# Kernel tuning notes

Measured on AMD Instinct MI355X. Metric: run time of the kernel, lower is better.

Reference implementation:

```python
import jax, jax.numpy as jnp
import numpy as np

B, S, H, L, V = 128, 512, 1024, 4, 32000


def setup_inputs() -> dict:
    key = jax.random.key(0)
    ks = jax.random.split(key, 7)
    lengths = jax.random.randint(ks[0], (B,), 1, S + 1)
    lengths = lengths.at[0].set(S)  # force max length == S so T is static
    tok = jax.random.randint(ks[1], (B, S), 1, V)  # nonzero tokens inside length
    pos = jnp.arange(S)[None, :]
    x = jnp.where(pos < lengths[:, None], tok, 0)  # 0 = pad (x>0 defines length)
    emb = jax.random.normal(ks[2], (V, H), dtype=jnp.float32) * 0.02
    W_ih = jax.random.normal(ks[3], (L, 4 * H, H), dtype=jnp.float32) / np.float32(np.sqrt(H))
    W_hh = jax.random.normal(ks[4], (L, 4 * H, H), dtype=jnp.float32) / np.float32(np.sqrt(H))
    b_ih = jax.random.normal(ks[5], (L, 4 * H), dtype=jnp.float32) * 0.01
    b_hh = jax.random.normal(ks[6], (L, 4 * H), dtype=jnp.float32) * 0.01
    return {"x": x, "emb": emb, "W_ih": W_ih, "W_hh": W_hh, "b_ih": b_ih, "b_hh": b_hh}


def reference(x, emb, W_ih, W_hh, b_ih, b_hh):
    # lengths and pack's descending sort (pack_padded_sequence, enforce_sorted=False)
    lengths = jnp.sum(x > 0, axis=1)                         # [B]
    sorted_idx = jnp.argsort(-lengths, stable=True)          # sorted (desc) order
    unsort_idx = jnp.argsort(sorted_idx)                     # packed.unsorted_indices

    # Source bug: `start` is never advanced, so every iteration runs a ONE-step
    # stacked LSTM (zero init state) on packed.data[0:bs_t] == t=0 embeddings of
    # the bs_t longest sequences. Compute that single step once on all rows.
    xt = emb[x[sorted_idx, 0]]                               # [B, H] sorted order
    h0 = jnp.zeros_like(xt)                                  # zero initial hidden
    hs, cs = [], []
    for l in range(W_ih.shape[0]):
        gates = xt @ W_ih[l].T + b_ih[l] + h0 @ W_hh[l].T + b_hh[l]
        i, f, g, o = jnp.split(gates, 4, axis=-1)            # torch LSTMCell order
        c = jax.nn.sigmoid(i) * jnp.tanh(g)                  # f * c0 = 0
        h = jax.nn.sigmoid(o) * jnp.tanh(c)
        xt = h
        hs.append(h)
        cs.append(c)

    # output[t, b] = top-layer h for original seq b, zeroed where t >= lengths[b]
    T = x.shape[1]                                           # max length == S
    h_top = xt[unsort_idx]                                   # back to original order
    tmask = (jnp.arange(T)[:, None] < lengths[None, :]).astype(h_top.dtype)  # [T,B]
    output = tmask[:, :, None] * h_top[None, :, :]           # [T, B, H]

    # state from the LAST loop iteration: sorted order, rows >= bs_last zero-padded
    bs_last = jnp.sum(lengths >= T)                          # batch size at t = T-1
    smask = (jnp.arange(x.shape[0]) < bs_last).astype(h_top.dtype)[None, :, None]
    state_h = jnp.stack(hs, axis=0) * smask                  # [L, B, H]
    state_c = jnp.stack(cs, axis=0) * smask                  # [L, B, H]
    return output, state_h, state_c
```

## Files before the change

kernel.cpp:

```cpp
#include <hip/hip_runtime.h>

#define Bn 128
#define Sn 512
#define Hn 1024
#define Ln 4

typedef float nfloat4 __attribute__((ext_vector_type(4)));

__device__ __forceinline__ float sigmoidf_(float x) { return 1.0f / (1.0f + __expf(-x)); }

__global__ __launch_bounds__(1024) void lensort_kernel(const int* __restrict__ x,
                                                       int* __restrict__ lengths,
                                                       int* __restrict__ rank,
                                                       int* __restrict__ tok_sorted,
                                                       int* __restrict__ bs_last) {
  __shared__ int pc[128][8];
  __shared__ int sl[128];
  __shared__ int cnt;
  const int t = threadIdx.x;
  const int row = t >> 3, seg = t & 7;
  int c = 0;
  const int4* xp = (const int4*)x + row * 128 + seg * 16;
#pragma unroll
  for (int i = 0; i < 16; i++) {
    int4 v = xp[i];
    c += (v.x > 0) + (v.y > 0) + (v.z > 0) + (v.w > 0);
  }
  pc[row][seg] = c;
  if (t == 0) cnt = 0;
  __syncthreads();
  int len = 0;
  if (t < 128) {
#pragma unroll
    for (int i = 0; i < 8; i++) len += pc[t][i];
    sl[t] = len;
    lengths[t] = len;
  }
  __syncthreads();
  if (t < 128) {
    int r = 0;
    for (int b2 = 0; b2 < 128; b2++) {
      int l2 = sl[b2];
      r += (l2 > len) || (l2 == len && b2 < t);
    }
    rank[t] = r;
    tok_sorted[r] = x[t * Sn];
    if (len >= Sn) atomicAdd(&cnt, 1);
  }
  __syncthreads();
  if (t == 0) bs_last[0] = cnt;
}

__global__ __launch_bounds__(320) void gemm_kernel(const float* __restrict__ xt,
                                                   const int* __restrict__ tok,
                                                   const float* __restrict__ Wl,
                                                   float* __restrict__ part,
                                                   const int* __restrict__ lengths,
                                                   float* __restrict__ out,
                                                   const int layer) {
  __shared__ float xtT[32][132];
  __shared__ float Ws[32][96];
  __shared__ int sTok[128];
  const int t = threadIdx.x;
  const int mtile = blockIdx.x & 31;
  const int kc = blockIdx.x >> 5;

  if (tok != nullptr) {
    if (t < 128) sTok[t] = tok[t];
    __syncthreads();
  }

  if (t >= 256) {
    const int lane = t - 256;
    const int b = blockIdx.x & 127;
    const int half = blockIdx.x >> 7;
    const int len = lengths[b];
    const int tw0 = 32 + layer * 120 + half * 60;
    const nfloat4 z = (nfloat4)0.0f;
#pragma unroll
    for (int tile = 0; tile < 4; tile++) {
      __builtin_amdgcn_s_barrier();
      const int r0 = tw0 + tile * 15;
      for (int i = 0; i < 15; i++) {
        const int tt = r0 + i;
        if (tt >= len) {
          nfloat4* p = (nfloat4*)out + ((size_t)tt * 128 + b) * 256 + lane * 4;
          __builtin_nontemporal_store(z, p + 0);
          __builtin_nontemporal_store(z, p + 1);
          __builtin_nontemporal_store(z, p + 2);
          __builtin_nontemporal_store(z, p + 3);
        }
      }
      __builtin_amdgcn_s_barrier();
    }
    return;
  }

  const int rg = t & 31;
  const int msub = t >> 5;
  const int k0 = kc * 128;
  const int kv4 = (t & 7) * 4;

  const float* xrow[4];
#pragma unroll
  for (int i = 0; i < 4; i++) {
    const int r = i * 32 + (t >> 3);
    const int row = (tok != nullptr) ? sTok[r] : r;
    xrow[i] = xt + (size_t)row * 1024;
  }

  float acc[3][4][4];
#pragma unroll
  for (int q = 0; q < 3; q++)
#pragma unroll
    for (int mm = 0; mm < 4; mm++)
#pragma unroll
      for (int rr = 0; rr < 4; rr++) acc[q][mm][rr] = 0.0f;

  float4 xreg[4], wreg[3];
  {
#pragma unroll
    for (int i = 0; i < 4; i++) xreg[i] = *(const float4*)&xrow[i][k0 + kv4];
#pragma unroll
    for (int i = 0; i < 3; i++) {
      int jj = i * 32 + (t >> 3);
      int q = jj >> 5, mloc = jj & 31;
      int qoff = (q == 0) ? 0 : ((q == 1) ? 2048 : 3072);
      wreg[i] = *(const float4*)&Wl[(size_t)(qoff + mtile * 32 + mloc) * 1024 + k0 + kv4];
    }
  }

#pragma unroll
  for (int tile = 0; tile < 4; tile++) {
    __syncthreads();
#pragma unroll
    for (int i = 0; i < 4; i++) {
      const int r = i * 32 + (t >> 3);
      xtT[kv4 + 0][r] = xreg[i].x;
      xtT[kv4 + 1][r] = xreg[i].y;
      xtT[kv4 + 2][r] = xreg[i].z;
      xtT[kv4 + 3][r] = xreg[i].w;
    }
#pragma unroll
    for (int i = 0; i < 3; i++) {
      const int jj = i * 32 + (t >> 3);
      Ws[kv4 + 0][jj] = wreg[i].x;
      Ws[kv4 + 1][jj] = wreg[i].y;
      Ws[kv4 + 2][jj] = wreg[i].z;
      Ws[kv4 + 3][jj] = wreg[i].w;
    }
    float4 xnxt[4], wnxt[3];
    if (tile < 3) {
      const int kt = k0 + (tile + 1) * 32;
#pragma unroll
      for (int i = 0; i < 4; i++) xnxt[i] = *(const float4*)&xrow[i][kt + kv4];
#pragma unroll
      for (int i = 0; i < 3; i++) {
        int jj = i * 32 + (t >> 3);
        int q = jj >> 5, mloc = jj & 31;
        int qoff = (q == 0) ? 0 : ((q == 1) ? 2048 : 3072);
        wnxt[i] = *(const float4*)&Wl[(size_t)(qoff + mtile * 32 + mloc) * 1024 + kt + kv4];
      }
    }
    __syncthreads();
#pragma unroll
    for (int kk = 0; kk < 32; kk++) {
      const float4 xv = *(const float4*)&xtT[kk][rg * 4];
      const float4 w0 = *(const float4*)&Ws[kk][msub * 4];
      const float4 w1 = *(const float4*)&Ws[kk][32 + msub * 4];
      const float4 w2 = *(const float4*)&Ws[kk][64 + msub * 4];
      const float xa[4] = {xv.x, xv.y, xv.z, xv.w};
      const float wv[3][4] = {{w0.x, w0.y, w0.z, w0.w},
                              {w1.x, w1.y, w1.z, w1.w},
                              {w2.x, w2.y, w2.z, w2.w}};
#pragma unroll
      for (int q = 0; q < 3; q++)
#pragma unroll
        for (int mm = 0; mm < 4; mm++)
#pragma unroll
          for (int rr = 0; rr < 4; rr++)
            acc[q][mm][rr] = fmaf(wv[q][mm], xa[rr], acc[q][mm][rr]);
    }
    if (tile < 3) {
#pragma unroll
      for (int i = 0; i < 4; i++) xreg[i] = xnxt[i];
#pragma unroll
      for (int i = 0; i < 3; i++) wreg[i] = wnxt[i];
    }
  }

  const int mbase = mtile * 32 + msub * 4;
#pragma unroll
  for (int q = 0; q < 3; q++)
#pragma unroll
    for (int mm = 0; mm < 4; mm++) {
      float4 v = make_float4(acc[q][mm][0], acc[q][mm][1], acc[q][mm][2], acc[q][mm][3]);
      *(float4*)&part[(((size_t)kc * 3 + q) * 1024 + (mbase + mm)) * 128 + rg * 4] = v;
    }
}

__global__ __launch_bounds__(128) void act_kernel(const float* __restrict__ part,
                                                  const float* __restrict__ bih,
                                                  const float* __restrict__ bhh,
                                                  const int* __restrict__ bs_last,
                                                  float* __restrict__ xt_out,
                                                  float* __restrict__ sh,
                                                  float* __restrict__ sc) {
  const int r = threadIdx.x;
  const int m0 = blockIdx.x * 4;
  const int bs = bs_last[0];
  float hv[4], cv[4];
#pragma unroll
  for (int mm = 0; mm < 4; mm++) {
    const int m = m0 + mm;
    float si = 0.f, sg = 0.f, so = 0.f;
#pragma unroll
    for (int kc = 0; kc < 8; kc++) {
      const float* p = part + (((size_t)kc * 3) * 1024 + m) * 128 + r;
      si += p[0];
      sg += p[(size_t)1024 * 128];
      so += p[(size_t)2048 * 128];
    }
    si += bih[m] + bhh[m];
    sg += bih[2048 + m] + bhh[2048 + m];
    so += bih[3072 + m] + bhh[3072 + m];
    const float c = sigmoidf_(si) * tanhf(sg);
    const float h = sigmoidf_(so) * tanhf(c);
    hv[mm] = h;
    cv[mm] = c;
  }
  const float msk = (r < bs) ? 1.0f : 0.0f;
  *(float4*)&xt_out[(size_t)r * 1024 + m0] = make_float4(hv[0], hv[1], hv[2], hv[3]);
  *(float4*)&sh[(size_t)r * 1024 + m0] =
      make_float4(msk * hv[0], msk * hv[1], msk * hv[2], msk * hv[3]);
  *(float4*)&sc[(size_t)r * 1024 + m0] =
      make_float4(msk * cv[0], msk * cv[1], msk * cv[2], msk * cv[3]);
}

__global__ __launch_bounds__(256) void bcast_kernel(const float* __restrict__ hfin,
                                                    const int* __restrict__ lengths,
                                                    const int* __restrict__ rank,
                                                    float* __restrict__ out) {
  const int b = blockIdx.x & 127;
  const int c = blockIdx.x >> 7;
  const int len = lengths[b];
  const int t0 = c * 64;
  if (t0 < len) {
    const nfloat4 v = ((const nfloat4*)hfin)[rank[b] * 256 + threadIdx.x];
    const int hi = (len < t0 + 64) ? len : (t0 + 64);
    nfloat4* p = (nfloat4*)out + ((size_t)t0 * 128 + b) * 256 + threadIdx.x;
    for (int tt = t0; tt < hi; tt++) {
      __builtin_nontemporal_store(v, p);
      p += 32768;
    }
  }
  if (c == 0 && len < 32) {
    const nfloat4 z = (nfloat4)0.0f;
    nfloat4* pz = (nfloat4*)out + ((size_t)len * 128 + b) * 256 + threadIdx.x;
    for (int tt = len; tt < 32; tt++) {
      __builtin_nontemporal_store(z, pz);
      pz += 32768;
    }
  }
}

extern "C" void kernel_launch(void* const* d_in, const int* in_sizes, int n_in,
                              void* d_out, int out_size, void* d_ws, size_t ws_size,
                              hipStream_t stream) {
  const int* x = (const int*)d_in[0];
  const float* emb = (const float*)d_in[1];
  const float* W_ih = (const float*)d_in[2];
  const float* b_ih = (const float*)d_in[4];
  const float* b_hh = (const float*)d_in[5];

  float* out = (float*)d_out;
  float* sh = out + (size_t)Sn * Bn * Hn;
  float* sc = sh + (size_t)Ln * Bn * Hn;
  float* part = out;

  char* ws = (char*)d_ws;
  int* lengths = (int*)ws;
  int* rank = lengths + 128;
  int* tok_sorted = rank + 128;
  int* bs_last = tok_sorted + 128;
  float* xtA = (float*)(ws + 4096);
  float* xtB = xtA + 128 * 1024;

  lensort_kernel<<<1, 1024, 0, stream>>>(x, lengths, rank, tok_sorted, bs_last);

  float* bufs[2] = {xtA, xtB};
  const float* xin = emb;
  const int* tokp = tok_sorted;
  for (int l = 0; l < Ln; l++) {
    gemm_kernel<<<256, 320, 0, stream>>>(xin, tokp, W_ih + (size_t)l * 4 * Hn * Hn, part,
                                         lengths, out, l);
    act_kernel<<<256, 128, 0, stream>>>(part, b_ih + l * 4 * Hn, b_hh + l * 4 * Hn, bs_last,
                                        bufs[l & 1], sh + (size_t)l * Bn * Hn,
                                        sc + (size_t)l * Bn * Hn);
    xin = bufs[l & 1];
    tokp = nullptr;
  }
  bcast_kernel<<<1024, 256, 0, stream>>>(xin, lengths, rank, out);
}
```

Before: 544.2 us.

## Fuse LSTM gate activation into GEMM via grid barrier and move padding zeros to broadcast

```diff
diff --git a/kernel.cpp b/kernel.cpp
--- a/kernel.cpp
+++ b/kernel.cpp
@@ -13,10 +13,11 @@
                                                        int* __restrict__ lengths,
                                                        int* __restrict__ rank,
                                                        int* __restrict__ tok_sorted,
-                                                       int* __restrict__ bs_last) {
+                                                       int* __restrict__ bs_last,
+                                                       int* __restrict__ cnt) {
   __shared__ int pc[128][8];
   __shared__ int sl[128];
-  __shared__ int cnt;
+  __shared__ int scnt;
   const int t = threadIdx.x;
   const int row = t >> 3, seg = t & 7;
   int c = 0;
@@ -27,7 +28,8 @@
     c += (v.x > 0) + (v.y > 0) + (v.z > 0) + (v.w > 0);
   }
   pc[row][seg] = c;
-  if (t == 0) cnt = 0;
+  if (t == 0) scnt = 0;
+  if (t < 4) cnt[t] = 0;
   __syncthreads();
   int len = 0;
   if (t < 128) {
@@ -45,61 +47,39 @@
     }
     rank[t] = r;
     tok_sorted[r] = x[t * Sn];
-    if (len >= Sn) atomicAdd(&cnt, 1);
-  }
-  __syncthreads();
-  if (t == 0) bs_last[0] = cnt;
-}
-
-__global__ __launch_bounds__(320) void gemm_kernel(const float* __restrict__ xt,
-                                                   const int* __restrict__ tok,
-                                                   const float* __restrict__ Wl,
-                                                   float* __restrict__ part,
-                                                   const int* __restrict__ lengths,
-                                                   float* __restrict__ out,
-                                                   const int layer) {
+    if (len >= Sn) atomicAdd(&scnt, 1);
+  }
+  __syncthreads();
+  if (t == 0) bs_last[0] = scnt;
+}
+
+__global__ __launch_bounds__(256) void gemm_fused(const float* __restrict__ xt,
+                                                  const int* __restrict__ tok,
+                                                  const float* __restrict__ Wl,
+                                                  float* __restrict__ part,
+                                                  const float* __restrict__ bih,
+                                                  const float* __restrict__ bhh,
+                                                  const int* __restrict__ bs_last,
+                                                  int* __restrict__ cnt,
+                                                  float* __restrict__ xt_out,
+                                                  float* __restrict__ sh,
+                                                  float* __restrict__ sc) {
   __shared__ float xtT[32][132];
   __shared__ float Ws[32][96];
   __shared__ int sTok[128];
+  __shared__ float red[128][12];
   const int t = threadIdx.x;
   const int mtile = blockIdx.x & 31;
   const int kc = blockIdx.x >> 5;
-
-  if (tok != nullptr) {
-    if (t < 128) sTok[t] = tok[t];
-    __syncthreads();
-  }
-
-  if (t >= 256) {
-    const int lane = t - 256;
-    const int b = blockIdx.x & 127;
-    const int half = blockIdx.x >> 7;
-    const int len = lengths[b];
-    const int tw0 = 32 + layer * 120 + half * 60;
-    const nfloat4 z = (nfloat4)0.0f;
-#pragma unroll
-    for (int tile = 0; tile < 4; tile++) {
-      __builtin_amdgcn_s_barrier();
-      const int r0 = tw0 + tile * 15;
-      for (int i = 0; i < 15; i++) {
-        const int tt = r0 + i;
-        if (tt >= len) {
-          nfloat4* p = (nfloat4*)out + ((size_t)tt * 128 + b) * 256 + lane * 4;
-          __builtin_nontemporal_store(z, p + 0);
-          __builtin_nontemporal_store(z, p + 1);
-          __builtin_nontemporal_store(z, p + 2);
-          __builtin_nontemporal_store(z, p + 3);
-        }
-      }
-      __builtin_amdgcn_s_barrier();
-    }
-    return;
-  }
-
   const int rg = t & 31;
   const int msub = t >> 5;
   const int k0 = kc * 128;
   const int kv4 = (t & 7) * 4;
+
+  if (tok != nullptr) {
+    if (t < 128) sTok[t] = tok[t];
+    __syncthreads();
+  }
 
   const float* xrow[4];
 #pragma unroll
@@ -197,44 +177,61 @@
       float4 v = make_float4(acc[q][mm][0], acc[q][mm][1], acc[q][mm][2], acc[q][mm][3]);
       *(float4*)&part[(((size_t)kc * 3 + q) * 1024 + (mbase + mm)) * 128 + rg * 4] = v;
     }
-}
-
-__global__ __launch_bounds__(128) void act_kernel(const float* __restrict__ part,
-                                                  const float* __restrict__ bih,
-                                                  const float* __restrict__ bhh,
-                                                  const int* __restrict__ bs_last,
-                                                  float* __restrict__ xt_out,
-                                                  float* __restrict__ sh,
-                                                  float* __restrict__ sc) {
-  const int r = threadIdx.x;
+
+  __threadfence();
+  __syncthreads();
+  if (t == 0) {
+    atomicAdd(cnt, 1);
+    while (__hip_atomic_load(cnt, __ATOMIC_RELAXED, __HIP_MEMORY_SCOPE_AGENT) < 256) {}
+  }
+  __syncthreads();
+  __threadfence();
+
+  const int r = t & 127;
+  const int half = t >> 7;
   const int m0 = blockIdx.x * 4;
-  const int bs = bs_last[0];
-  float hv[4], cv[4];
-#pragma unroll
-  for (int mm = 0; mm < 4; mm++) {
-    const int m = m0 + mm;
-    float si = 0.f, sg = 0.f, so = 0.f;
-#pragma unroll
-    for (int kc = 0; kc < 8; kc++) {
-      const float* p = part + (((size_t)kc * 3) * 1024 + m) * 128 + r;
-      si += p[0];
-      sg += p[(size_t)1024 * 128];
-      so += p[(size_t)2048 * 128];
-    }
-    si += bih[m] + bhh[m];
-    sg += bih[2048 + m] + bhh[2048 + m];
-    so += bih[3072 + m] + bhh[3072 + m];
-    const float c = sigmoidf_(si) * tanhf(sg);
-    const float h = sigmoidf_(so) * tanhf(c);
-    hv[mm] = h;
-    cv[mm] = c;
-  }
-  const float msk = (r < bs) ? 1.0f : 0.0f;
-  *(float4*)&xt_out[(size_t)r * 1024 + m0] = make_float4(hv[0], hv[1], hv[2], hv[3]);
-  *(float4*)&sh[(size_t)r * 1024 + m0] =
-      make_float4(msk * hv[0], msk * hv[1], msk * hv[2], msk * hv[3]);
-  *(float4*)&sc[(size_t)r * 1024 + m0] =
-      make_float4(msk * cv[0], msk * cv[1], msk * cv[2], msk * cv[3]);
+  float s[3][4];
+#pragma unroll
+  for (int q = 0; q < 3; q++)
+#pragma unroll
+    for (int mm = 0; mm < 4; mm++) s[q][mm] = 0.0f;
+#pragma unroll
+  for (int k4 = 0; k4 < 4; k4++) {
+    const int kcc = half * 4 + k4;
+#pragma unroll
+    for (int q = 0; q < 3; q++)
+#pragma unroll
+      for (int mm = 0; mm < 4; mm++)
+        s[q][mm] += part[(((size_t)kcc * 3 + q) * 1024 + (m0 + mm)) * 128 + r];
+  }
+  if (half == 1) {
+#pragma unroll
+    for (int q = 0; q < 3; q++)
+#pragma unroll
+      for (int mm = 0; mm < 4; mm++) red[r][q * 4 + mm] = s[q][mm];
+  }
+  __syncthreads();
+  if (half == 0) {
+    const int bs = bs_last[0];
+    float hv[4], cv[4];
+#pragma unroll
+    for (int mm = 0; mm < 4; mm++) {
+      const int m = m0 + mm;
+      const float si = s[0][mm] + red[r][0 * 4 + mm] + bih[m] + bhh[m];
+      const float sg = s[1][mm] + red[r][1 * 4 + mm] + bih[2048 + m] + bhh[2048 + m];
+      const float so = s[2][mm] + red[r][2 * 4 + mm] + bih[3072 + m] + bhh[3072 + m];
+      const float c = sigmoidf_(si) * tanhf(sg);
+      const float h = sigmoidf_(so) * tanhf(c);
+      hv[mm] = h;
+      cv[mm] = c;
+    }
+    const float msk = (r < bs) ? 1.0f : 0.0f;
+    *(float4*)&xt_out[(size_t)r * 1024 + m0] = make_float4(hv[0], hv[1], hv[2], hv[3]);
+    *(float4*)&sh[(size_t)r * 1024 + m0] =
+        make_float4(msk * hv[0], msk * hv[1], msk * hv[2], msk * hv[3]);
+    *(float4*)&sc[(size_t)r * 1024 + m0] =
+        make_float4(msk * cv[0], msk * cv[1], msk * cv[2], msk * cv[3]);
+  }
 }
 
 __global__ __launch_bounds__(256) void bcast_kernel(const float* __restrict__ hfin,
@@ -245,22 +242,19 @@
   const int c = blockIdx.x >> 7;
   const int len = lengths[b];
   const int t0 = c * 64;
-  if (t0 < len) {
-    const nfloat4 v = ((const nfloat4*)hfin)[rank[b] * 256 + threadIdx.x];
-    const int hi = (len < t0 + 64) ? len : (t0 + 64);
-    nfloat4* p = (nfloat4*)out + ((size_t)t0 * 128 + b) * 256 + threadIdx.x;
-    for (int tt = t0; tt < hi; tt++) {
-      __builtin_nontemporal_store(v, p);
-      p += 32768;
-    }
-  }
-  if (c == 0 && len < 32) {
-    const nfloat4 z = (nfloat4)0.0f;
-    nfloat4* pz = (nfloat4*)out + ((size_t)len * 128 + b) * 256 + threadIdx.x;
-    for (int tt = len; tt < 32; tt++) {
-      __builtin_nontemporal_store(z, pz);
-      pz += 32768;
-    }
+  nfloat4 v = (nfloat4)0.0f;
+  if (t0 < len) v = ((const nfloat4*)hfin)[rank[b] * 256 + threadIdx.x];
+  int valid = len - t0;
+  valid = valid < 0 ? 0 : (valid > 64 ? 64 : valid);
+  nfloat4* p = (nfloat4*)out + ((size_t)t0 * 128 + b) * 256 + threadIdx.x;
+  for (int i = 0; i < valid; i++) {
+    __builtin_nontemporal_store(v, p);
+    p += 32768;
+  }
+  const nfloat4 z = (nfloat4)0.0f;
+  for (int i = valid; i < 64; i++) {
+    __builtin_nontemporal_store(z, p);
+    p += 32768;
   }
 }
 
@@ -283,19 +277,19 @@
   int* rank = lengths + 128;
   int* tok_sorted = rank + 128;
   int* bs_last = tok_sorted + 128;
+  int* cnt = bs_last + 1;
   float* xtA = (float*)(ws + 4096);
   float* xtB = xtA + 128 * 1024;
 
-  lensort_kernel<<<1, 1024, 0, stream>>>(x, lengths, rank, tok_sorted, bs_last);
+  lensort_kernel<<<1, 1024, 0, stream>>>(x, lengths, rank, tok_sorted, bs_last, cnt);
 
   float* bufs[2] = {xtA, xtB};
   const float* xin = emb;
   const int* tokp = tok_sorted;
   for (int l = 0; l < Ln; l++) {
-    gemm_kernel<<<256, 320, 0, stream>>>(xin, tokp, W_ih + (size_t)l * 4 * Hn * Hn, part,
-                                         lengths, out, l);
-    act_kernel<<<256, 128, 0, stream>>>(part, b_ih + l * 4 * Hn, b_hh + l * 4 * Hn, bs_last,
-                                        bufs[l & 1], sh + (size_t)l * Bn * Hn,
+    gemm_fused<<<256, 256, 0, stream>>>(xin, tokp, W_ih + (size_t)l * 4 * Hn * Hn, part,
+                                        b_ih + l * 4 * Hn, b_hh + l * 4 * Hn, bs_last,
+                                        cnt + l, bufs[l & 1], sh + (size_t)l * Bn * Hn,
                                         sc + (size_t)l * Bn * Hn);
     xin = bufs[l & 1];
     tokp = nullptr;
```

Result: slower. 726.0 us (+33.4%).
